# Kernel optimization log

Hardware: AMD Instinct MI355X
Metric: run time of the kernel (lower is better)

The kernel has to match this reference:

```python
import jax, jax.numpy as jnp
import numpy as np

D_MODEL, N_HEADS, D_HEAD, D_MLP = 768, 12, 64, 3072
BATCH, SEQ = 2, 2048
EPS = 1e-5
IGNORE = -100000.0
INIT = 0.02


def gelu_new(x):
    # GPT-2 tanh-approx GELU
    c = jnp.sqrt(2.0 / jnp.pi).astype(x.dtype)
    return 0.5 * x * (1.0 + jnp.tanh(c * (x + 0.044715 * x ** 3)))


def layer_norm(x, w, b):
    x = x - jnp.mean(x, axis=-1, keepdims=True)
    scale = jnp.sqrt(jnp.mean(x * x, axis=-1, keepdims=True) + EPS)
    return (x / scale) * w + b


def setup_inputs() -> dict:
    key = jax.random.key(0)
    ks = jax.random.split(key, 8)
    f32 = jnp.float32
    return {
        "resid_pre": jax.random.normal(ks[0], (BATCH, SEQ, D_MODEL), f32),
        "W_Q": INIT * jax.random.normal(ks[1], (N_HEADS, D_MODEL, D_HEAD), f32),
        "b_Q": jnp.zeros((N_HEADS, D_HEAD), f32),
        "W_K": INIT * jax.random.normal(ks[2], (N_HEADS, D_MODEL, D_HEAD), f32),
        "b_K": jnp.zeros((N_HEADS, D_HEAD), f32),
        "W_V": INIT * jax.random.normal(ks[3], (N_HEADS, D_MODEL, D_HEAD), f32),
        "b_V": jnp.zeros((N_HEADS, D_HEAD), f32),
        "W_O": INIT * jax.random.normal(ks[4], (N_HEADS, D_HEAD, D_MODEL), f32),
        "b_O": jnp.zeros((D_MODEL,), f32),
        "ln1_w": jnp.ones((D_MODEL,), f32),
        "ln1_b": jnp.zeros((D_MODEL,), f32),
        "ln2_w": jnp.ones((D_MODEL,), f32),
        "ln2_b": jnp.zeros((D_MODEL,), f32),
        "W_in": INIT * jax.random.normal(ks[5], (D_MODEL, D_MLP), f32),
        "b_in": jnp.zeros((D_MLP,), f32),
        "W_out": INIT * jax.random.normal(ks[6], (D_MLP, D_MODEL), f32),
        "b_out": jnp.zeros((D_MODEL,), f32),
    }


def reference(resid_pre, W_Q, b_Q, W_K, b_K, W_V, b_V, W_O, b_O,
              ln1_w, ln1_b, ln2_w, ln2_b, W_in, b_in, W_out, b_out):
    x = layer_norm(resid_pre, ln1_w, ln1_b)
    # per-head projections: [batch, pos, heads, d_head]
    q = jnp.einsum('bsd,hde->bshe', x, W_Q) + b_Q
    k = jnp.einsum('bsd,hde->bshe', x, W_K) + b_K
    v = jnp.einsum('bsd,hde->bshe', x, W_V) + b_V
    scores = jnp.einsum('bqhe,bkhe->bhqk', q, k) / jnp.sqrt(jnp.float32(D_HEAD))
    S = scores.shape[-1]
    causal = jnp.triu(jnp.ones((S, S), bool), k=1)
    scores = jnp.where(causal, jnp.float32(IGNORE), scores)
    pattern = jax.nn.softmax(scores, axis=-1)
    z = jnp.einsum('bhqk,bkhe->bqhe', pattern, v)
    attn_out = jnp.einsum('bqhe,hed->bqd', z, W_O) + b_O
    resid_mid = resid_pre + attn_out
    y = layer_norm(resid_mid, ln2_w, ln2_b)
    mlp_out = jnp.einsum('bsd,dm->bsm', y, W_in) + b_in
    mlp_out = gelu_new(mlp_out)
    mlp_out = jnp.einsum('bsm,md->bsd', mlp_out, W_out) + b_out
    return resid_mid + mlp_out
```

## Files before the change

### kernel.cpp

```cpp
#include <hip/hip_runtime.h>
#include <hip/hip_bf16.h>

#define SEQ   2048
#define DMODEL 768
#define NHEADS 12
#define DHEAD  64
#define DMLP  3072
#define TTOK  4096
#define EPSLN 1e-5f

typedef unsigned short u16;
typedef __attribute__((ext_vector_type(4))) float f32x4;
typedef __attribute__((ext_vector_type(8))) short s16x8;
typedef __attribute__((ext_vector_type(8))) unsigned short u16x8;
typedef __attribute__((ext_vector_type(4))) unsigned short u16x4;

__device__ __forceinline__ float bf2f(u16 u) {
    return __uint_as_float(((unsigned int)u) << 16);
}
__device__ __forceinline__ u16 f2bf(float f) {
    unsigned int x = __float_as_uint(f);
    return (u16)((x + 0x7FFFu + ((x >> 16) & 1u)) >> 16);
}
__device__ __forceinline__ bool is_bf16(const void* probe) {
    return ((const u16*)probe)[0] == 0x3F80u;
}
__device__ __forceinline__ float readIn(const void* p, long i, bool bf) {
    return bf ? bf2f(((const u16*)p)[i]) : ((const float*)p)[i];
}

__device__ __forceinline__ float gelu_new(float x) {
    float x3 = x * x * x;
    float u = 0.7978845608028654f * (x + 0.044715f * x3);
    return 0.5f * x * (1.0f + tanhf(u));
}

__device__ __forceinline__ void stage16(const u16* g, u16* l) {
    __builtin_amdgcn_global_load_lds(
        (const __attribute__((address_space(1))) void*)g,
        (__attribute__((address_space(3))) void*)l,
        16, 0, 0);
}

__global__ __launch_bounds__(256) void transpose_kernel(
    const void* __restrict__ src, u16* __restrict__ dst, int R, int C,
    const void* __restrict__ probe)
{
    bool bf = is_bf16(probe);
    __shared__ float t[32][33];
    size_t boff = (size_t)R * C * blockIdx.z;
    int r0 = blockIdx.y * 32, c0 = blockIdx.x * 32;
    int tx = threadIdx.x, ty = threadIdx.y;
#pragma unroll
    for (int i = 0; i < 4; i++) {
        int r = r0 + ty + i * 8;
        t[ty + i * 8][tx] = readIn(src, boff + (size_t)r * C + c0 + tx, bf);
    }
    __syncthreads();
#pragma unroll
    for (int i = 0; i < 4; i++) {
        int c = c0 + ty + i * 8;
        dst[boff + (size_t)c * R + r0 + tx] = f2bf(t[tx][ty + i * 8]);
    }
}

__global__ __launch_bounds__(256) void vec_repack(
    const void* bq, const void* bk, const void* bv, const void* bo,
    const void* bin, const void* bout,
    const void* l1w, const void* l1b, const void* l2w, const void* l2b,
    float* __restrict__ bias_qkv, float* __restrict__ bias_o,
    float* __restrict__ bias_in, float* __restrict__ bias_out, float* __restrict__ lnv)
{
    bool bf = is_bf16(l1w);
    int tid = threadIdx.x;
    for (int i = tid; i < 768; i += 256) {
        bias_qkv[i]        = readIn(bq, i, bf);
        bias_qkv[768 + i]  = readIn(bk, i, bf);
        bias_qkv[1536 + i] = readIn(bv, i, bf);
        bias_o[i]   = readIn(bo, i, bf);
        bias_out[i] = readIn(bout, i, bf);
        lnv[i]        = readIn(l1w, i, bf);
        lnv[768 + i]  = readIn(l1b, i, bf);
        lnv[1536 + i] = readIn(l2w, i, bf);
        lnv[2304 + i] = readIn(l2b, i, bf);
    }
    for (int i = tid; i < 3072; i += 256) bias_in[i] = readIn(bin, i, bf);
}

template <bool PROBED>
__global__ __launch_bounds__(256) void ln_kernel(
    const void* __restrict__ in, const float* __restrict__ w, const float* __restrict__ b,
    u16* __restrict__ out, const void* __restrict__ probe)
{
    bool bf = PROBED ? is_bf16(probe) : false;
    int t = blockIdx.x;
    int tid = threadIdx.x;
    __shared__ float red[8];

    float v[3];
#pragma unroll
    for (int j = 0; j < 3; j++)
        v[j] = PROBED ? readIn(in, (long)t * DMODEL + tid + j * 256, bf)
                      : ((const float*)in)[(size_t)t * DMODEL + tid + j * 256];

    float s = v[0] + v[1] + v[2];
#pragma unroll
    for (int off = 1; off < 64; off <<= 1) s += __shfl_xor(s, off, 64);
    if ((tid & 63) == 0) red[tid >> 6] = s;
    __syncthreads();
    float mean = (red[0] + red[1] + red[2] + red[3]) * (1.0f / DMODEL);

    float sq = 0.0f;
#pragma unroll
    for (int j = 0; j < 3; j++) { v[j] -= mean; sq += v[j] * v[j]; }
#pragma unroll
    for (int off = 1; off < 64; off <<= 1) sq += __shfl_xor(sq, off, 64);
    if ((tid & 63) == 0) red[4 + (tid >> 6)] = sq;
    __syncthreads();
    float var = (red[4] + red[5] + red[6] + red[7]) * (1.0f / DMODEL);
    float inv = rsqrtf(var + EPSLN);

#pragma unroll
    for (int j = 0; j < 3; j++) {
        int c = tid + j * 256;
        out[(size_t)t * DMODEL + c] = f2bf(v[j] * inv * w[c] + b[c]);
    }
}

template <int EPI, int BM>
__global__ __launch_bounds__(256) void mfma_gemm(
    const u16* __restrict__ A, const u16* __restrict__ Bt,
    const float* __restrict__ bias, const void* __restrict__ res,
    void* __restrict__ Cout, u16* __restrict__ Cout2,
    int M, int N, int K, const void* probe)
{
    constexpr int NI = BM / 32;
    __shared__ u16 As[4][BM][8];
    __shared__ u16 Bs[4][128][8];
    int tid = threadIdx.x, lane = tid & 63, w = tid >> 6;
    int m0 = blockIdx.y * BM, n0 = blockIdx.x * 128;
    int wr = (w & 1) * (BM / 2), wc = (w >> 1) * 64;
    int lm = lane & 15, quad = lane >> 4;

    const u16* gA = A  + (size_t)(m0 + lane) * K + w * 8;
    const u16* gB = Bt + (size_t)(n0 + lane) * K + w * 8;
    size_t rowK64 = (size_t)64 * K;

    f32x4 acc[NI][4];
    const f32x4 z4 = {0.f, 0.f, 0.f, 0.f};
#pragma unroll
    for (int i = 0; i < NI; i++)
#pragma unroll
        for (int j = 0; j < 4; j++) acc[i][j] = z4;

    for (int k0 = 0; k0 < K; k0 += 32) {
        stage16(gA + k0, &As[w][0][0]);
        if (BM == 128) stage16(gA + rowK64 + k0, &As[w][64][0]);
        stage16(gB + k0,          &Bs[w][0][0]);
        stage16(gB + rowK64 + k0, &Bs[w][64][0]);
        __syncthreads();

        s16x8 af[NI], bfr[4];
#pragma unroll
        for (int i = 0; i < NI; i++)
            af[i] = *(const s16x8*)&As[quad][wr + i * 16 + lm][0];
#pragma unroll
        for (int j = 0; j < 4; j++)
            bfr[j] = *(const s16x8*)&Bs[quad][wc + j * 16 + lm][0];
#pragma unroll
        for (int i = 0; i < NI; i++)
#pragma unroll
            for (int j = 0; j < 4; j++)
                acc[i][j] = __builtin_amdgcn_mfma_f32_16x16x32_bf16(
                    af[i], bfr[j], acc[i][j], 0, 0, 0);
        __syncthreads();
    }

    bool pbf = (EPI == 2 || EPI == 3) ? is_bf16(probe) : false;
#pragma unroll
    for (int i = 0; i < NI; i++) {
#pragma unroll
        for (int j = 0; j < 4; j++) {
            int col = n0 + wc + j * 16 + lm;
            float bsv = bias[col];
            int row0 = m0 + wr + i * 16 + quad * 4;
            if (EPI == 4) {
                if (col < 1536) {
#pragma unroll
                    for (int r = 0; r < 4; r++)
                        ((u16*)Cout)[(size_t)(row0 + r) * 1536 + col] = f2bf(acc[i][j][r] + bsv);
                } else {
                    int e9 = col - 1536, hh = e9 >> 6, ee = e9 & 63;
                    int bb = row0 >> 11, t0 = row0 & 2047;
                    u16x4 pv;
#pragma unroll
                    for (int r = 0; r < 4; r++) pv[r] = f2bf(acc[i][j][r] + bsv);
                    *(u16x4*)&Cout2[(((size_t)bb * 12 + hh) * 64 + ee) * 2048 + t0] = pv;
                }
            } else {
#pragma unroll
                for (int r = 0; r < 4; r++) {
                    size_t idx = (size_t)(row0 + r) * N + col;
                    float c = acc[i][j][r] + bsv;
                    if (EPI == 1) c = gelu_new(c);
                    if (EPI == 2) c += readIn(res, (long)idx, pbf);
                    if (EPI == 3) c += ((const float*)res)[idx];
                    if (EPI == 2) {
                        ((float*)Cout)[idx] = c;
                    } else if (EPI == 3) {
                        if (pbf) ((u16*)Cout)[idx] = f2bf(c);
                        else     ((float*)Cout)[idx] = c;
                    } else {
                        ((u16*)Cout)[idx] = f2bf(c);
                    }
                }
            }
        }
    }
}

__global__ __launch_bounds__(256) void attn_mfma(
    const u16* __restrict__ qk, const u16* __restrict__ vT, u16* __restrict__ z)
{
    __shared__ u16 Qs[64][72];
    __shared__ u16 Ks[64][72];
    __shared__ u16 Vt[64][72];
    __shared__ u16 Ps[4][16][72];

    int tid = threadIdx.x, lane = tid & 63, w = tid >> 6;
    int lm = lane & 15, quad = lane >> 4;
    int bh = blockIdx.x % 24;
    int qt = 31 - blockIdx.x / 24;
    int b = bh / 12, h = bh % 12;
    int q0 = qt * 64;

    int tr = tid >> 2, tcg = (tid & 3) * 16;
    const u16* qbase = qk + (size_t)(b * SEQ) * 1536 + h * 64;
    const u16* kbase = qbase + 768;
    const u16* vbase = vT + (size_t)bh * 64 * SEQ;

    {
        const u16* g = qbase + (size_t)(q0 + tr) * 1536 + tcg;
        *(u16x8*)&Qs[tr][tcg]     = *(const u16x8*)g;
        *(u16x8*)&Qs[tr][tcg + 8] = *(const u16x8*)(g + 8);
    }

    f32x4 oacc[4];
    const f32x4 z4 = {0.f, 0.f, 0.f, 0.f};
    float m_[4], l_[4];
#pragma unroll
    for (int g = 0; g < 4; g++) oacc[g] = z4;
#pragma unroll
    for (int r = 0; r < 4; r++) { m_[r] = -1e30f; l_[r] = 0.f; }

    for (int kt = 0; kt <= qt; kt++) {
        int k0 = kt * 64;
        __syncthreads();
        {
            const u16* gk = kbase + (size_t)(k0 + tr) * 1536 + tcg;
            *(u16x8*)&Ks[tr][tcg]     = *(const u16x8*)gk;
            *(u16x8*)&Ks[tr][tcg + 8] = *(const u16x8*)(gk + 8);
            const u16* gv = vbase + (size_t)tr * SEQ + k0 + tcg;
            *(u16x8*)&Vt[tr][tcg]     = *(const u16x8*)gv;
            *(u16x8*)&Vt[tr][tcg + 8] = *(const u16x8*)(gv + 8);
        }
        __syncthreads();

        f32x4 sacc[4];
#pragma unroll
        for (int g = 0; g < 4; g++) sacc[g] = z4;
#pragma unroll
        for (int c = 0; c < 2; c++) {
            s16x8 aq = *(const s16x8*)&Qs[w * 16 + lm][c * 32 + quad * 8];
#pragma unroll
            for (int g = 0; g < 4; g++) {
                s16x8 bk = *(const s16x8*)&Ks[g * 16 + lm][c * 32 + quad * 8];
                sacc[g] = __builtin_amdgcn_mfma_f32_16x16x32_bf16(aq, bk, sacc[g], 0, 0, 0);
            }
        }

#pragma unroll
        for (int r = 0; r < 4; r++) {
            float sr[4];
#pragma unroll
            for (int g = 0; g < 4; g++) sr[g] = sacc[g][r] * 0.125f;
            if (kt == qt) {
                int qrow = w * 16 + quad * 4 + r;
#pragma unroll
                for (int g = 0; g < 4; g++)
                    if (g * 16 + lm > qrow) sr[g] = -1e30f;
            }
            float rm = fmaxf(fmaxf(sr[0], sr[1]), fmaxf(sr[2], sr[3]));
#pragma unroll
            for (int x = 1; x < 16; x <<= 1) rm = fmaxf(rm, __shfl_xor(rm, x, 16));
            float nm = fmaxf(m_[r], rm);
            float corr = __expf(m_[r] - nm);
            float p0 = __expf(sr[0] - nm), p1 = __expf(sr[1] - nm);
            float p2 = __expf(sr[2] - nm), p3 = __expf(sr[3] - nm);
            float rs = p0 + p1 + p2 + p3;
#pragma unroll
            for (int x = 1; x < 16; x <<= 1) rs += __shfl_xor(rs, x, 16);
            l_[r] = l_[r] * corr + rs;
            m_[r] = nm;
#pragma unroll
            for (int g = 0; g < 4; g++) oacc[g][r] *= corr;
            Ps[w][quad * 4 + r][0 * 16 + lm]  = f2bf(p0);
            Ps[w][quad * 4 + r][1 * 16 + lm]  = f2bf(p1);
            Ps[w][quad * 4 + r][2 * 16 + lm]  = f2bf(p2);
            Ps[w][quad * 4 + r][3 * 16 + lm]  = f2bf(p3);
        }

#pragma unroll
        for (int c = 0; c < 2; c++) {
            s16x8 ap = *(const s16x8*)&Ps[w][lm][c * 32 + quad * 8];
#pragma unroll
            for (int g = 0; g < 4; g++) {
                s16x8 bv = *(const s16x8*)&Vt[g * 16 + lm][c * 32 + quad * 8];
                oacc[g] = __builtin_amdgcn_mfma_f32_16x16x32_bf16(ap, bv, oacc[g], 0, 0, 0);
            }
        }
    }

#pragma unroll
    for (int r = 0; r < 4; r++) {
        float inv = 1.0f / l_[r];
        int row = b * SEQ + q0 + w * 16 + quad * 4 + r;
#pragma unroll
        for (int g = 0; g < 4; g++)
            z[(size_t)row * DMODEL + h * 64 + g * 16 + lm] = f2bf(oacc[g][r] * inv);
    }
}

extern "C" void kernel_launch(void* const* d_in, const int* in_sizes, int n_in,
                              void* d_out, int out_size, void* d_ws, size_t ws_size,
                              hipStream_t stream)
{
    const void* resid_pre = d_in[0];
    const void* W_Q = d_in[1];  const void* b_Q = d_in[2];
    const void* W_K = d_in[3];  const void* b_K = d_in[4];
    const void* W_V = d_in[5];  const void* b_V = d_in[6];
    const void* W_O = d_in[7];  const void* b_O = d_in[8];
    const void* ln1_w = d_in[9];  const void* ln1_b = d_in[10];
    const void* ln2_w = d_in[11]; const void* ln2_b = d_in[12];
    const void* W_in = d_in[13];  const void* b_in = d_in[14];
    const void* W_out = d_in[15]; const void* b_out = d_in[16];

    float* ws = (float*)d_ws;
    float* resid_mid = ws;
    u16* qk     = (u16*)(ws + 3145728);
    u16* vT     = (u16*)(ws + 6291456);
    u16* x_ln1  = (u16*)(ws + 7864320);
    u16* h_mlp  = (u16*)(ws + 3145728);
    u16* z_buf  = (u16*)(ws + 9437184);
    u16* y_ln2  = z_buf;
    u16* WqkvT  = (u16*)(ws + 11010048);
    u16* WOT    = (u16*)(ws + 11894784);
    u16* WinT   = (u16*)(ws + 12189696);
    u16* WoutT  = (u16*)(ws + 13369344);
    float* bias_qkv = ws + 14548992;
    float* bias_o   = ws + 14551296;
    float* bias_in  = ws + 14552064;
    float* bias_out = ws + 14555136;
    float* lnv      = ws + 14555904;

    transpose_kernel<<<dim3(2, 24, 12), dim3(32, 8), 0, stream>>>(W_Q, WqkvT,              768, 64,   ln1_w);
    transpose_kernel<<<dim3(2, 24, 12), dim3(32, 8), 0, stream>>>(W_K, WqkvT + 768 * 768,  768, 64,   ln1_w);
    transpose_kernel<<<dim3(2, 24, 12), dim3(32, 8), 0, stream>>>(W_V, WqkvT + 1536 * 768, 768, 64,   ln1_w);
    transpose_kernel<<<dim3(24, 24, 1), dim3(32, 8), 0, stream>>>(W_O, WOT,                768, 768,  ln1_w);
    transpose_kernel<<<dim3(96, 24, 1), dim3(32, 8), 0, stream>>>(W_in, WinT,              768, 3072, ln1_w);
    transpose_kernel<<<dim3(24, 96, 1), dim3(32, 8), 0, stream>>>(W_out, WoutT,            3072, 768, ln1_w);
    vec_repack<<<1, 256, 0, stream>>>(b_Q, b_K, b_V, b_O, b_in, b_out,
                                      ln1_w, ln1_b, ln2_w, ln2_b,
                                      bias_qkv, bias_o, bias_in, bias_out, lnv);
    ln_kernel<true><<<TTOK, 256, 0, stream>>>(resid_pre, lnv, lnv + 768, x_ln1, ln1_w);
    mfma_gemm<4, 128><<<dim3(18, 32), 256, 0, stream>>>(
        x_ln1, WqkvT, bias_qkv, nullptr, qk, vT, TTOK, 2304, DMODEL, nullptr);
    attn_mfma<<<768, 256, 0, stream>>>(qk, vT, z_buf);
    mfma_gemm<2, 64><<<dim3(6, 64), 256, 0, stream>>>(
        z_buf, WOT, bias_o, resid_pre, resid_mid, nullptr, TTOK, DMODEL, DMODEL, ln1_w);
    ln_kernel<false><<<TTOK, 256, 0, stream>>>(resid_mid, lnv + 1536, lnv + 2304, y_ln2, nullptr);
    mfma_gemm<1, 128><<<dim3(24, 32), 256, 0, stream>>>(
        y_ln2, WinT, bias_in, nullptr, h_mlp, nullptr, TTOK, DMLP, DMODEL, nullptr);
    mfma_gemm<3, 64><<<dim3(6, 64), 256, 0, stream>>>(
        h_mlp, WoutT, bias_out, resid_mid, d_out, nullptr, TTOK, DMODEL, DMLP, ln1_w);
}
```

Measured before the change: 428.2 us.

## Merge weight repack launches, store resid_mid as bf16, retile GEMMs with BN template

Combines the six transpose launches and the bias/LN-vector repack into one kernel that dispatches on block index. The residual-mid buffer is now stored in bf16 instead of fp32, which halves its write and read traffic in the O-projection epilogue, LN2 and the final residual add, at the cost of some precision. The GEMM gains a BN template parameter and swaps grid axes so that M runs along x. Smaller tiles (64x128 for QKV, 64x64 for the O and output projections) raise block counts and occupancy.

```diff
diff --git a/kernel.cpp b/kernel.cpp
--- a/kernel.cpp
+++ b/kernel.cpp
@@ -42,57 +42,66 @@
         16, 0, 0);
 }
 
-__global__ __launch_bounds__(256) void transpose_kernel(
-    const void* __restrict__ src, u16* __restrict__ dst, int R, int C,
-    const void* __restrict__ probe)
-{
-    bool bf = is_bf16(probe);
-    __shared__ float t[32][33];
-    size_t boff = (size_t)R * C * blockIdx.z;
-    int r0 = blockIdx.y * 32, c0 = blockIdx.x * 32;
-    int tx = threadIdx.x, ty = threadIdx.y;
-#pragma unroll
-    for (int i = 0; i < 4; i++) {
-        int r = r0 + ty + i * 8;
-        t[ty + i * 8][tx] = readIn(src, boff + (size_t)r * C + c0 + tx, bf);
-    }
-    __syncthreads();
-#pragma unroll
-    for (int i = 0; i < 4; i++) {
-        int c = c0 + ty + i * 8;
-        dst[boff + (size_t)c * R + r0 + tx] = f2bf(t[tx][ty + i * 8]);
-    }
-}
-
-__global__ __launch_bounds__(256) void vec_repack(
+__global__ __launch_bounds__(256) void repack_all(
+    const void* W_O, const void* W_in, const void* W_out,
+    const void* W_Q, const void* W_K, const void* W_V,
     const void* bq, const void* bk, const void* bv, const void* bo,
     const void* bin, const void* bout,
     const void* l1w, const void* l1b, const void* l2w, const void* l2b,
+    u16* __restrict__ WOT, u16* __restrict__ WinT, u16* __restrict__ WoutT,
+    u16* __restrict__ WqkvT,
     float* __restrict__ bias_qkv, float* __restrict__ bias_o,
     float* __restrict__ bias_in, float* __restrict__ bias_out, float* __restrict__ lnv)
 {
     bool bf = is_bf16(l1w);
+    int id = blockIdx.x;
     int tid = threadIdx.x;
-    for (int i = tid; i < 768; i += 256) {
-        bias_qkv[i]        = readIn(bq, i, bf);
-        bias_qkv[768 + i]  = readIn(bk, i, bf);
-        bias_qkv[1536 + i] = readIn(bv, i, bf);
-        bias_o[i]   = readIn(bo, i, bf);
-        bias_out[i] = readIn(bout, i, bf);
-        lnv[i]        = readIn(l1w, i, bf);
-        lnv[768 + i]  = readIn(l1b, i, bf);
-        lnv[1536 + i] = readIn(l2w, i, bf);
-        lnv[2304 + i] = readIn(l2b, i, bf);
-    }
-    for (int i = tid; i < 3072; i += 256) bias_in[i] = readIn(bin, i, bf);
-}
-
-template <bool PROBED>
+    if (id == 6912) {
+        for (int i = tid; i < 768; i += 256) {
+            bias_qkv[i]        = readIn(bq, i, bf);
+            bias_qkv[768 + i]  = readIn(bk, i, bf);
+            bias_qkv[1536 + i] = readIn(bv, i, bf);
+            bias_o[i]   = readIn(bo, i, bf);
+            bias_out[i] = readIn(bout, i, bf);
+            lnv[i]        = readIn(l1w, i, bf);
+            lnv[768 + i]  = readIn(l1b, i, bf);
+            lnv[1536 + i] = readIn(l2w, i, bf);
+            lnv[2304 + i] = readIn(l2b, i, bf);
+        }
+        for (int i = tid; i < 3072; i += 256) bias_in[i] = readIn(bin, i, bf);
+        return;
+    }
+    const void* src; u16* dst; int R, C, tr, tc;
+    size_t srcOff = 0, dstOff = 0;
+    if (id < 576)       { src = W_O;  dst = WOT;  R = 768;  C = 768;  tr = id / 24;  tc = id % 24; }
+    else if (id < 2880) { int j = id - 576;  src = W_in;  dst = WinT;  R = 768;  C = 3072; tr = j / 96; tc = j % 96; }
+    else if (id < 5184) { int j = id - 2880; src = W_out; dst = WoutT; R = 3072; C = 768;  tr = j / 24; tc = j % 24; }
+    else {
+        int j = id - 5184;
+        int q = j / 576, rem = j % 576, h = rem / 48, t = rem % 48;
+        src = (q == 0) ? W_Q : (q == 1) ? W_K : W_V;
+        dst = WqkvT; R = 768; C = 64; tr = t / 2; tc = t % 2;
+        srcOff = (size_t)h * 49152;
+        dstOff = ((size_t)q * 768 + h * 64) * 768;
+    }
+    __shared__ float tb[32][33];
+    int tx = tid & 31, ty = tid >> 5;
+    int r0 = tr * 32, c0 = tc * 32;
+#pragma unroll
+    for (int i = 0; i < 4; i++)
+        tb[ty + i * 8][tx] = readIn(src, srcOff + (size_t)(r0 + ty + i * 8) * C + c0 + tx, bf);
+    __syncthreads();
+#pragma unroll
+    for (int i = 0; i < 4; i++)
+        dst[dstOff + (size_t)(c0 + ty + i * 8) * R + r0 + tx] = f2bf(tb[tx][ty + i * 8]);
+}
+
+template <int MODE>
 __global__ __launch_bounds__(256) void ln_kernel(
     const void* __restrict__ in, const float* __restrict__ w, const float* __restrict__ b,
     u16* __restrict__ out, const void* __restrict__ probe)
 {
-    bool bf = PROBED ? is_bf16(probe) : false;
+    bool bf = (MODE == 0) ? is_bf16(probe) : true;
     int t = blockIdx.x;
     int tid = threadIdx.x;
     __shared__ float red[8];
@@ -100,8 +109,7 @@
     float v[3];
 #pragma unroll
     for (int j = 0; j < 3; j++)
-        v[j] = PROBED ? readIn(in, (long)t * DMODEL + tid + j * 256, bf)
-                      : ((const float*)in)[(size_t)t * DMODEL + tid + j * 256];
+        v[j] = readIn(in, (long)t * DMODEL + tid + j * 256, bf);
 
     float s = v[0] + v[1] + v[2];
 #pragma unroll
@@ -127,7 +135,7 @@
     }
 }
 
-template <int EPI, int BM>
+template <int EPI, int BM, int BN>
 __global__ __launch_bounds__(256) void mfma_gemm(
     const u16* __restrict__ A, const u16* __restrict__ Bt,
     const float* __restrict__ bias, const void* __restrict__ res,
@@ -135,42 +143,43 @@
     int M, int N, int K, const void* probe)
 {
     constexpr int NI = BM / 32;
+    constexpr int NJ = BN / 32;
     __shared__ u16 As[4][BM][8];
-    __shared__ u16 Bs[4][128][8];
+    __shared__ u16 Bs[4][BN][8];
     int tid = threadIdx.x, lane = tid & 63, w = tid >> 6;
-    int m0 = blockIdx.y * BM, n0 = blockIdx.x * 128;
-    int wr = (w & 1) * (BM / 2), wc = (w >> 1) * 64;
+    int m0 = blockIdx.x * BM, n0 = blockIdx.y * BN;
+    int wr = (w & 1) * (BM / 2), wc = (w >> 1) * (BN / 2);
     int lm = lane & 15, quad = lane >> 4;
 
     const u16* gA = A  + (size_t)(m0 + lane) * K + w * 8;
     const u16* gB = Bt + (size_t)(n0 + lane) * K + w * 8;
     size_t rowK64 = (size_t)64 * K;
 
-    f32x4 acc[NI][4];
+    f32x4 acc[NI][NJ];
     const f32x4 z4 = {0.f, 0.f, 0.f, 0.f};
 #pragma unroll
     for (int i = 0; i < NI; i++)
 #pragma unroll
-        for (int j = 0; j < 4; j++) acc[i][j] = z4;
+        for (int j = 0; j < NJ; j++) acc[i][j] = z4;
 
     for (int k0 = 0; k0 < K; k0 += 32) {
         stage16(gA + k0, &As[w][0][0]);
         if (BM == 128) stage16(gA + rowK64 + k0, &As[w][64][0]);
-        stage16(gB + k0,          &Bs[w][0][0]);
-        stage16(gB + rowK64 + k0, &Bs[w][64][0]);
+        stage16(gB + k0, &Bs[w][0][0]);
+        if (BN == 128) stage16(gB + rowK64 + k0, &Bs[w][64][0]);
         __syncthreads();
 
-        s16x8 af[NI], bfr[4];
+        s16x8 af[NI], bfr[NJ];
 #pragma unroll
         for (int i = 0; i < NI; i++)
             af[i] = *(const s16x8*)&As[quad][wr + i * 16 + lm][0];
 #pragma unroll
-        for (int j = 0; j < 4; j++)
+        for (int j = 0; j < NJ; j++)
             bfr[j] = *(const s16x8*)&Bs[quad][wc + j * 16 + lm][0];
 #pragma unroll
         for (int i = 0; i < NI; i++)
 #pragma unroll
-            for (int j = 0; j < 4; j++)
+            for (int j = 0; j < NJ; j++)
                 acc[i][j] = __builtin_amdgcn_mfma_f32_16x16x32_bf16(
                     af[i], bfr[j], acc[i][j], 0, 0, 0);
         __syncthreads();
@@ -180,7 +189,7 @@
 #pragma unroll
     for (int i = 0; i < NI; i++) {
 #pragma unroll
-        for (int j = 0; j < 4; j++) {
+        for (int j = 0; j < NJ; j++) {
             int col = n0 + wc + j * 16 + lm;
             float bsv = bias[col];
             int row0 = m0 + wr + i * 16 + quad * 4;
@@ -204,10 +213,8 @@
                     float c = acc[i][j][r] + bsv;
                     if (EPI == 1) c = gelu_new(c);
                     if (EPI == 2) c += readIn(res, (long)idx, pbf);
-                    if (EPI == 3) c += ((const float*)res)[idx];
-                    if (EPI == 2) {
-                        ((float*)Cout)[idx] = c;
-                    } else if (EPI == 3) {
+                    if (EPI == 3) c += bf2f(((const u16*)res)[idx]);
+                    if (EPI == 3) {
                         if (pbf) ((u16*)Cout)[idx] = f2bf(c);
                         else     ((float*)Cout)[idx] = c;
                     } else {
@@ -346,41 +353,38 @@
     const void* W_out = d_in[15]; const void* b_out = d_in[16];
 
     float* ws = (float*)d_ws;
-    float* resid_mid = ws;
-    u16* qk     = (u16*)(ws + 3145728);
-    u16* vT     = (u16*)(ws + 6291456);
-    u16* x_ln1  = (u16*)(ws + 7864320);
-    u16* h_mlp  = (u16*)(ws + 3145728);
-    u16* z_buf  = (u16*)(ws + 9437184);
-    u16* y_ln2  = z_buf;
-    u16* WqkvT  = (u16*)(ws + 11010048);
-    u16* WOT    = (u16*)(ws + 11894784);
-    u16* WinT   = (u16*)(ws + 12189696);
-    u16* WoutT  = (u16*)(ws + 13369344);
-    float* bias_qkv = ws + 14548992;
-    float* bias_o   = ws + 14551296;
-    float* bias_in  = ws + 14552064;
-    float* bias_out = ws + 14555136;
-    float* lnv      = ws + 14555904;
-
-    transpose_kernel<<<dim3(2, 24, 12), dim3(32, 8), 0, stream>>>(W_Q, WqkvT,              768, 64,   ln1_w);
-    transpose_kernel<<<dim3(2, 24, 12), dim3(32, 8), 0, stream>>>(W_K, WqkvT + 768 * 768,  768, 64,   ln1_w);
-    transpose_kernel<<<dim3(2, 24, 12), dim3(32, 8), 0, stream>>>(W_V, WqkvT + 1536 * 768, 768, 64,   ln1_w);
-    transpose_kernel<<<dim3(24, 24, 1), dim3(32, 8), 0, stream>>>(W_O, WOT,                768, 768,  ln1_w);
-    transpose_kernel<<<dim3(96, 24, 1), dim3(32, 8), 0, stream>>>(W_in, WinT,              768, 3072, ln1_w);
-    transpose_kernel<<<dim3(24, 96, 1), dim3(32, 8), 0, stream>>>(W_out, WoutT,            3072, 768, ln1_w);
-    vec_repack<<<1, 256, 0, stream>>>(b_Q, b_K, b_V, b_O, b_in, b_out,
-                                      ln1_w, ln1_b, ln2_w, ln2_b,
-                                      bias_qkv, bias_o, bias_in, bias_out, lnv);
-    ln_kernel<true><<<TTOK, 256, 0, stream>>>(resid_pre, lnv, lnv + 768, x_ln1, ln1_w);
-    mfma_gemm<4, 128><<<dim3(18, 32), 256, 0, stream>>>(
+    u16* qk        = (u16*)(ws);
+    u16* vT        = (u16*)(ws + 3145728);
+    u16* x_ln1     = (u16*)(ws + 4718592);
+    u16* h_mlp     = (u16*)(ws);
+    u16* z_buf     = (u16*)(ws + 6291456);
+    u16* y_ln2     = z_buf;
+    u16* resid_mid = (u16*)(ws + 7864320);
+    u16* WqkvT     = (u16*)(ws + 9437184);
+    u16* WOT       = (u16*)(ws + 10321920);
+    u16* WinT      = (u16*)(ws + 10616832);
+    u16* WoutT     = (u16*)(ws + 11796480);
+    float* bias_qkv = ws + 12976128;
+    float* bias_o   = ws + 12978432;
+    float* bias_in  = ws + 12979200;
+    float* bias_out = ws + 12982272;
+    float* lnv      = ws + 12983040;
+
+    repack_all<<<6913, 256, 0, stream>>>(
+        W_O, W_in, W_out, W_Q, W_K, W_V,
+        b_Q, b_K, b_V, b_O, b_in, b_out,
+        ln1_w, ln1_b, ln2_w, ln2_b,
+        WOT, WinT, WoutT, WqkvT,
+        bias_qkv, bias_o, bias_in, bias_out, lnv);
+    ln_kernel<0><<<TTOK, 256, 0, stream>>>(resid_pre, lnv, lnv + 768, x_ln1, ln1_w);
+    mfma_gemm<4, 64, 128><<<dim3(64, 18), 256, 0, stream>>>(
         x_ln1, WqkvT, bias_qkv, nullptr, qk, vT, TTOK, 2304, DMODEL, nullptr);
     attn_mfma<<<768, 256, 0, stream>>>(qk, vT, z_buf);
-    mfma_gemm<2, 64><<<dim3(6, 64), 256, 0, stream>>>(
+    mfma_gemm<2, 64, 64><<<dim3(64, 12), 256, 0, stream>>>(
         z_buf, WOT, bias_o, resid_pre, resid_mid, nullptr, TTOK, DMODEL, DMODEL, ln1_w);
-    ln_kernel<false><<<TTOK, 256, 0, stream>>>(resid_mid, lnv + 1536, lnv + 2304, y_ln2, nullptr);
-    mfma_gemm<1, 128><<<dim3(24, 32), 256, 0, stream>>>(
+    ln_kernel<2><<<TTOK, 256, 0, stream>>>(resid_mid, lnv + 1536, lnv + 2304, y_ln2, nullptr);
+    mfma_gemm<1, 128, 128><<<dim3(32, 24), 256, 0, stream>>>(
         y_ln2, WinT, bias_in, nullptr, h_mlp, nullptr, TTOK, DMLP, DMODEL, nullptr);
-    mfma_gemm<3, 64><<<dim3(6, 64), 256, 0, stream>>>(
+    mfma_gemm<3, 64, 64><<<dim3(64, 12), 256, 0, stream>>>(
         h_mlp, WoutT, bias_out, resid_mid, d_out, nullptr, TTOK, DMODEL, DMLP, ln1_w);
 }
```

Result: faster. 403.6 us (-5.7%).
